# Performance work log

Hardware: AMD Instinct MI355X
Metric: run time of the kernel (lower is better)

Reference implementation:

```python
import jax, jax.numpy as jnp
import numpy as np

B, S, D, H = 2, 2048, 1024, 16
DK = D // H

def setup_inputs() -> dict:
    key = jax.random.key(0)
    ks = jax.random.split(key, 9)
    scale = 1.0 / np.sqrt(D)
    return {
        "x": jax.random.normal(ks[0], (B, S, D), dtype=jnp.float32),
        "Wq": jax.random.uniform(ks[1], (D, D), jnp.float32, -scale, scale),
        "bq": jax.random.uniform(ks[2], (D,), jnp.float32, -scale, scale),
        "Wk": jax.random.uniform(ks[3], (D, D), jnp.float32, -scale, scale),
        "bk": jax.random.uniform(ks[4], (D,), jnp.float32, -scale, scale),
        "Wv": jax.random.uniform(ks[5], (D, D), jnp.float32, -scale, scale),
        "bv": jax.random.uniform(ks[6], (D,), jnp.float32, -scale, scale),
        "Wo": jax.random.uniform(ks[7], (D, D), jnp.float32, -scale, scale),
        "bo": jax.random.uniform(ks[8], (D,), jnp.float32, -scale, scale),
    }

def reference(x, Wq, bq, Wk, bk, Wv, bv, Wo, bo):
    # QKV projections (torch Linear: x @ W.T + b)
    q = x @ Wq.T + bq
    k = x @ Wk.T + bk
    v = x @ Wv.T + bv
    # [B, H, S, DK]
    q = q.reshape(B, S, H, DK).transpose(0, 2, 1, 3)
    k = k.reshape(B, S, H, DK).transpose(0, 2, 1, 3)
    v = v.reshape(B, S, H, DK).transpose(0, 2, 1, 3)
    scores = jnp.einsum('bhqd,bhkd->bhqk', q, k) / jnp.sqrt(jnp.float32(DK))
    p = jax.nn.softmax(scores, axis=-1)  # dropout is identity in eval mode
    o = jnp.einsum('bhqk,bhkd->bhqd', p, v)
    o = o.transpose(0, 2, 1, 3).reshape(B, S, D)
    return o @ Wo.T + bo
```

## Files before the change

kernel.cpp:

```cpp
#include <hip/hip_runtime.h>
#include <hip/hip_bf16.h>


typedef __attribute__((ext_vector_type(8))) short short8;
typedef __attribute__((ext_vector_type(4))) short short4v;
typedef __attribute__((ext_vector_type(4))) float f32x4;
typedef __attribute__((ext_vector_type(8))) unsigned short u16x8;
typedef __attribute__((ext_vector_type(2))) unsigned int u32x2;

__device__ __forceinline__ unsigned short f2bf(float f) {
    unsigned int u = __builtin_bit_cast(unsigned int, f);
    u += 0x7FFFu + ((u >> 16) & 1u);
    return (unsigned short)(u >> 16);
}

__device__ __forceinline__ unsigned short bfc(float f) {
    return __builtin_bit_cast(unsigned short, __float2bfloat16(f));
}

__device__ __forceinline__ float exp2_fast(float x) {
    return __builtin_amdgcn_exp2f(x);
}

__device__ __forceinline__ void gload16(const void* gsrc, void* ldst) {
    __builtin_amdgcn_global_load_lds(
        (const __attribute__((address_space(1))) unsigned int*)gsrc,
        (__attribute__((address_space(3))) unsigned int*)ldst, 16, 0, 0);
}

__global__ void cast_all(const float* __restrict__ x,
                         const float* __restrict__ wq, const float* __restrict__ wk,
                         const float* __restrict__ wv, const float* __restrict__ wo,
                         unsigned short* __restrict__ xb,
                         unsigned short* __restrict__ wqb, unsigned short* __restrict__ wkb,
                         unsigned short* __restrict__ wvb, unsigned short* __restrict__ wob)
{
    const int z = blockIdx.y;
    const float* src; unsigned short* dst; int n4;
    if (z == 0)      { src = x;  dst = xb;  n4 = 4096 * 1024 / 4; }
    else if (z == 1) { src = wq; dst = wqb; n4 = 1024 * 1024 / 4; }
    else if (z == 2) { src = wk; dst = wkb; n4 = 1024 * 1024 / 4; }
    else if (z == 3) { src = wv; dst = wvb; n4 = 1024 * 1024 / 4; }
    else             { src = wo; dst = wob; n4 = 1024 * 1024 / 4; }
    int i = blockIdx.x * blockDim.x + threadIdx.x;
    if (i < n4) {
        float4 v = reinterpret_cast<const float4*>(src)[i];
        ushort4 o;
        o.x = f2bf(v.x); o.y = f2bf(v.y); o.z = f2bf(v.z); o.w = f2bf(v.w);
        reinterpret_cast<ushort4*>(dst)[i] = o;
    }
}

__global__ __launch_bounds__(256, 2)
void qkv_gemm(const unsigned short* __restrict__ A,
              const unsigned short* __restrict__ Wq_,
              const unsigned short* __restrict__ Wk_,
              const unsigned short* __restrict__ Wv_,
              const float* __restrict__ bq_,
              const float* __restrict__ bk_,
              const float* __restrict__ bv_,
              unsigned short* __restrict__ Qb,
              unsigned short* __restrict__ Kb,
              unsigned short* __restrict__ Vtb)
{
    const int K = 1024;
    __shared__ __align__(16) unsigned short As[128][64];
    __shared__ __align__(16) unsigned short Bs[128][64];

    const int z = blockIdx.z;
    const unsigned short* Bw = (z == 0) ? Wq_ : (z == 1) ? Wk_ : Wv_;
    const float* bias = (z == 0) ? bq_ : (z == 1) ? bk_ : bv_;
    unsigned short* dst = (z == 0) ? Qb : (z == 1) ? Kb : Vtb;
    const float alpha = (z == 0) ? 0.125f * 1.44269504088896340736f : 1.0f;

    const int tid  = threadIdx.x;
    const int lane = tid & 63;
    const int wave = tid >> 6;
    const int wm = (wave >> 1) * 64;
    const int wn = (wave & 1) * 64;
    const int rowBase = blockIdx.y * 128;
    const int colBase = blockIdx.x * 128;
    const int l15 = lane & 15;
    const int lg  = lane >> 4;

    const int srow   = lane >> 3;
    const int schunk = lane & 7;
    const int gchunk = schunk ^ srow;

    f32x4 acc[4][4] = {};

    for (int kt = 0; kt < K; kt += 64) {
        __syncthreads();
#pragma unroll
        for (int it = 0; it < 4; ++it) {
            int r = wave * 8 + it * 32 + srow;
            gload16(A  + (size_t)(rowBase + r) * K + kt + gchunk * 8, &As[wave * 8 + it * 32][0]);
            gload16(Bw + (size_t)(colBase + r) * K + kt + gchunk * 8, &Bs[wave * 8 + it * 32][0]);
        }
        __syncthreads();
#pragma unroll
        for (int kk = 0; kk < 2; ++kk) {
            short8 af[4], bf[4];
#pragma unroll
            for (int fm = 0; fm < 4; ++fm) {
                int r  = wm + fm * 16 + l15;
                int kb = (kk * 4 + lg) ^ (r & 7);
                af[fm] = *reinterpret_cast<const short8*>(&As[r][kb * 8]);
            }
#pragma unroll
            for (int fn = 0; fn < 4; ++fn) {
                int r  = wn + fn * 16 + l15;
                int kb = (kk * 4 + lg) ^ (r & 7);
                bf[fn] = *reinterpret_cast<const short8*>(&Bs[r][kb * 8]);
            }
#pragma unroll
            for (int fm = 0; fm < 4; ++fm)
#pragma unroll
                for (int fn = 0; fn < 4; ++fn)
                    acc[fm][fn] = __builtin_amdgcn_mfma_f32_16x16x32_bf16(
                        af[fm], bf[fn], acc[fm][fn], 0, 0, 0);
        }
    }

#pragma unroll
    for (int fm = 0; fm < 4; ++fm)
#pragma unroll
        for (int fn = 0; fn < 4; ++fn)
#pragma unroll
            for (int r = 0; r < 4; ++r) {
                int grow = rowBase + wm + fm * 16 + lg * 4 + r;
                int gcol = colBase + wn + fn * 16 + l15;
                float v = (acc[fm][fn][r] + bias[gcol]) * alpha;
                int b = grow >> 11, s = grow & 2047;
                int h = gcol >> 6,  dk = gcol & 63;
                if (z < 2)
                    dst[(((size_t)b * 16 + h) * 2048 + s) * 64 + dk] = f2bf(v);
                else
                    dst[(((size_t)b * 16 + h) * 64 + dk) * 2048 + s] = f2bf(v);
            }
}

__global__ __launch_bounds__(256, 2)
void gemm_out(const unsigned short* __restrict__ A,
              const unsigned short* __restrict__ Bw,
              const float* __restrict__ bias,
              float* __restrict__ Cout, int M, int N, int K)
{
    __shared__ __align__(16) unsigned short As[128][64];
    __shared__ __align__(16) unsigned short Bs[64][64];

    const int tid  = threadIdx.x;
    const int lane = tid & 63;
    const int wave = tid >> 6;
    const int wm = (wave >> 1) * 64;
    const int wn = (wave & 1) * 32;
    const int rowBase = blockIdx.y * 128;
    const int colBase = blockIdx.x * 64;
    const int l15 = lane & 15;
    const int lg  = lane >> 4;

    const int srow   = lane >> 3;
    const int schunk = lane & 7;
    const int gchunk = schunk ^ srow;

    f32x4 acc[4][2] = {};

    for (int kt = 0; kt < K; kt += 64) {
        __syncthreads();
#pragma unroll
        for (int it = 0; it < 4; ++it) {
            int r = wave * 8 + it * 32 + srow;
            gload16(A + (size_t)(rowBase + r) * K + kt + gchunk * 8, &As[wave * 8 + it * 32][0]);
        }
#pragma unroll
        for (int it = 0; it < 2; ++it) {
            int rb = wave * 16 + it * 8;
            int r  = rb + srow;
            gload16(Bw + (size_t)(colBase + r) * K + kt + gchunk * 8, &Bs[rb][0]);
        }
        __syncthreads();
#pragma unroll
        for (int kk = 0; kk < 2; ++kk) {
            short8 af[4], bf[2];
#pragma unroll
            for (int fm = 0; fm < 4; ++fm) {
                int r  = wm + fm * 16 + l15;
                int kb = (kk * 4 + lg) ^ (r & 7);
                af[fm] = *reinterpret_cast<const short8*>(&As[r][kb * 8]);
            }
#pragma unroll
            for (int fn = 0; fn < 2; ++fn) {
                int r  = wn + fn * 16 + l15;
                int kb = (kk * 4 + lg) ^ (r & 7);
                bf[fn] = *reinterpret_cast<const short8*>(&Bs[r][kb * 8]);
            }
#pragma unroll
            for (int fm = 0; fm < 4; ++fm)
#pragma unroll
                for (int fn = 0; fn < 2; ++fn)
                    acc[fm][fn] = __builtin_amdgcn_mfma_f32_16x16x32_bf16(
                        af[fm], bf[fn], acc[fm][fn], 0, 0, 0);
        }
    }

#pragma unroll
    for (int fm = 0; fm < 4; ++fm)
#pragma unroll
        for (int fn = 0; fn < 2; ++fn)
#pragma unroll
            for (int r = 0; r < 4; ++r) {
                int grow = rowBase + wm + fm * 16 + lg * 4 + r;
                int gcol = colBase + wn + fn * 16 + l15;
                Cout[(size_t)grow * N + gcol] = acc[fm][fn][r] + bias[gcol];
            }
}

__global__ __launch_bounds__(256, 2)
void attn_kernel(const unsigned short* __restrict__ Q,
                 const unsigned short* __restrict__ Kt,
                 const unsigned short* __restrict__ Vt,
                 unsigned short* __restrict__ O)
{
    __shared__ __align__(16) unsigned short Ks[2][128][64];
    __shared__ __align__(16) unsigned short Vs[2][64][128];
    __shared__ __align__(16) unsigned short Ps[4][32][64];

    const int lid = blockIdx.x + 16 * blockIdx.y;
    const int bh  = 4 * (lid & 7) + ((lid >> 3) & 3);
    const int qt  = lid >> 5;
    const int tid  = threadIdx.x;
    const int lane = tid & 63;
    const int w    = tid >> 6;
    const int l15 = lane & 15;
    const int lg  = lane >> 4;

    const unsigned short* Qbh = Q  + (size_t)bh * 2048 * 64;
    const unsigned short* Kbh = Kt + (size_t)bh * 2048 * 64;
    const unsigned short* Vbh = Vt + (size_t)bh * 64 * 2048;

    short8 qf[2][2];
#pragma unroll
    for (int fq = 0; fq < 2; ++fq)
#pragma unroll
        for (int kk = 0; kk < 2; ++kk) {
            int row = qt * 128 + w * 32 + fq * 16 + l15;
            qf[fq][kk] = *reinterpret_cast<const short8*>(
                Qbh + (size_t)row * 64 + kk * 32 + lg * 8);
        }

    short8 ones;
#pragma unroll
    for (int j = 0; j < 8; ++j) ones[j] = (short)0x3F80;

    f32x4 accO[2][4] = {};
    f32x4 accSum[2] = {};

    const int sr  = tid >> 3, skb = tid & 7;
    const int vr  = tid >> 4, vkb = tid & 15;

    unsigned short* PsW = &Ps[w][0][0];

    u16x8 kst[4], vst[4];
#pragma unroll
    for (int it = 0; it < 4; ++it)
        kst[it] = *reinterpret_cast<const u16x8*>(Kbh + (size_t)(sr + it * 32) * 64 + skb * 8);
#pragma unroll
    for (int it = 0; it < 4; ++it)
        vst[it] = *reinterpret_cast<const u16x8*>(Vbh + (size_t)(vr + it * 16) * 2048 + vkb * 8);

    int cur = 0;
    for (int t = 0; t < 16; ++t) {
#pragma unroll
        for (int it = 0; it < 4; ++it) {
            int r = sr + it * 32;
            *reinterpret_cast<u16x8*>(&Ks[cur][r][(skb ^ (r & 7)) * 8]) = kst[it];
        }
#pragma unroll
        for (int it = 0; it < 4; ++it) {
            int r = vr + it * 16;
            *reinterpret_cast<u16x8*>(&Vs[cur][r][(vkb ^ (r & 15)) * 8]) = vst[it];
        }
        __syncthreads();

        if (t < 15) {
#pragma unroll
            for (int it = 0; it < 4; ++it)
                kst[it] = *reinterpret_cast<const u16x8*>(
                    Kbh + (size_t)((t + 1) * 128 + sr + it * 32) * 64 + skb * 8);
#pragma unroll
            for (int it = 0; it < 4; ++it)
                vst[it] = *reinterpret_cast<const u16x8*>(
                    Vbh + (size_t)(vr + it * 16) * 2048 + (t + 1) * 128 + vkb * 8);
        }

        f32x4 accS[8][2] = {};
#pragma unroll
        for (int kk = 0; kk < 2; ++kk) {
            short8 kf[8];
#pragma unroll
            for (int fk = 0; fk < 8; ++fk) {
                int r  = fk * 16 + l15;
                int kb = (kk * 4 + lg) ^ (r & 7);
                kf[fk] = *reinterpret_cast<const short8*>(&Ks[cur][r][kb * 8]);
            }
#pragma unroll
            for (int fk = 0; fk < 8; ++fk)
#pragma unroll
                for (int fq = 0; fq < 2; ++fq)
                    accS[fk][fq] = __builtin_amdgcn_mfma_f32_16x16x32_bf16(
                        kf[fk], qf[fq][kk], accS[fk][fq], 0, 0, 0);
        }

#pragma unroll
        for (int hh = 0; hh < 2; ++hh) {
#pragma unroll
            for (int fq = 0; fq < 2; ++fq) {
                const int ql = fq * 16 + l15;
#pragma unroll
                for (int f2 = 0; f2 < 4; ++f2) {
                    int fk = hh * 4 + f2;
                    float p0 = exp2_fast(accS[fk][fq][0]);
                    float p1 = exp2_fast(accS[fk][fq][1]);
                    float p2 = exp2_fast(accS[fk][fq][2]);
                    float p3 = exp2_fast(accS[fk][fq][3]);
                    unsigned int lo = (unsigned int)bfc(p0) | ((unsigned int)bfc(p1) << 16);
                    unsigned int hi = (unsigned int)bfc(p2) | ((unsigned int)bfc(p3) << 16);
                    u32x2 tmp; tmp.x = lo; tmp.y = hi;
                    short4v pk = __builtin_bit_cast(short4v, tmp);
                    int c = (f2 * 2 + (lg >> 1)) ^ (ql & 7);
                    *reinterpret_cast<short4v*>(
                        reinterpret_cast<char*>(PsW) + ql * 128 + c * 16 + (lg & 1) * 8) = pk;
                }
            }
            asm volatile("" ::: "memory");

#pragma unroll
            for (int k2 = 0; k2 < 2; ++k2) {
                short8 pf[2], vf[4];
#pragma unroll
                for (int fq = 0; fq < 2; ++fq) {
                    int ql = fq * 16 + l15;
                    int c  = (k2 * 4 + lg) ^ (ql & 7);
                    pf[fq] = *reinterpret_cast<const short8*>(
                        reinterpret_cast<char*>(PsW) + ql * 128 + c * 16);
                }
#pragma unroll
                for (int fd = 0; fd < 4; ++fd) {
                    int row = fd * 16 + l15;
                    int kb  = ((hh * 2 + k2) * 4 + lg) ^ (row & 15);
                    vf[fd] = *reinterpret_cast<const short8*>(&Vs[cur][row][kb * 8]);
                }
#pragma unroll
                for (int fq = 0; fq < 2; ++fq) {
#pragma unroll
                    for (int fd = 0; fd < 4; ++fd)
                        accO[fq][fd] = __builtin_amdgcn_mfma_f32_16x16x32_bf16(
                            pf[fq], vf[fd], accO[fq][fd], 0, 0, 0);
                    accSum[fq] = __builtin_amdgcn_mfma_f32_16x16x32_bf16(
                        pf[fq], ones, accSum[fq], 0, 0, 0);
                }
            }
            asm volatile("" ::: "memory");
        }

        cur ^= 1;
    }

    const int b = bh >> 4, h = bh & 15;
#pragma unroll
    for (int fq = 0; fq < 2; ++fq)
#pragma unroll
        for (int r = 0; r < 4; ++r) {
            float linv = 1.0f / accSum[fq][r];
            int s = qt * 128 + w * 32 + fq * 16 + lg * 4 + r;
#pragma unroll
            for (int fd = 0; fd < 4; ++fd) {
                int dk = fd * 16 + l15;
                O[((size_t)b * 2048 + s) * 1024 + h * 64 + dk] = f2bf(accO[fq][fd][r] * linv);
            }
        }
}

extern "C" void kernel_launch(void* const* d_in, const int* in_sizes, int n_in,
                              void* d_out, int out_size, void* d_ws, size_t ws_size,
                              hipStream_t stream)
{
    const float* x  = (const float*)d_in[0];
    const float* Wq = (const float*)d_in[1];
    const float* bq = (const float*)d_in[2];
    const float* Wk = (const float*)d_in[3];
    const float* bk = (const float*)d_in[4];
    const float* Wv = (const float*)d_in[5];
    const float* bv = (const float*)d_in[6];
    const float* Wo = (const float*)d_in[7];
    const float* bo = (const float*)d_in[8];
    float* out = (float*)d_out;

    char* ws = (char*)d_ws;
    unsigned short* xb  = (unsigned short*)(ws);
    unsigned short* wqb = (unsigned short*)(ws + ((size_t)8  << 20));
    unsigned short* wkb = (unsigned short*)(ws + ((size_t)10 << 20));
    unsigned short* wvb = (unsigned short*)(ws + ((size_t)12 << 20));
    unsigned short* wob = (unsigned short*)(ws + ((size_t)14 << 20));
    unsigned short* Qb  = (unsigned short*)(ws + ((size_t)16 << 20));
    unsigned short* Kb  = (unsigned short*)(ws + ((size_t)24 << 20));
    unsigned short* Vtb = (unsigned short*)(ws + ((size_t)32 << 20));
    unsigned short* Ob  = (unsigned short*)(ws + ((size_t)40 << 20));

    cast_all<<<dim3(4096, 5), 256, 0, stream>>>(x, Wq, Wk, Wv, Wo,
                                                xb, wqb, wkb, wvb, wob);

    qkv_gemm<<<dim3(8, 32, 3), 256, 0, stream>>>(xb, wqb, wkb, wvb, bq, bk, bv,
                                                 Qb, Kb, Vtb);

    attn_kernel<<<dim3(16, 32), 256, 0, stream>>>(Qb, Kb, Vtb, Ob);

    gemm_out<<<dim3(16, 32), 256, 0, stream>>>(Ob, wob, bo, out, 4096, 1024, 1024);
}
```

Baseline: 113.4 us.

## Split attention KV range in two and merge partials in a reduce kernel

The attention grid gains a z-dimension of 2, so each block processes half of the key/value tiles. It writes unnormalized bf16 partial outputs and row sums to the workspace, and a new reduce kernel adds the two halves and normalizes before the output projection. This doubles the number of blocks to improve CU occupancy and parallelism. The K/V LDS staging drops from double-buffered to single-buffered with an extra barrier. The price is an additional kernel launch, extra global traffic for the partials, and bf16 rounding of unnormalized partials.

```diff
diff --git a/kernel.cpp b/kernel.cpp
--- a/kernel.cpp
+++ b/kernel.cpp
@@ -12,6 +12,11 @@
     unsigned int u = __builtin_bit_cast(unsigned int, f);
     u += 0x7FFFu + ((u >> 16) & 1u);
     return (unsigned short)(u >> 16);
+}
+
+__device__ __forceinline__ float bf2f(unsigned short u) {
+    unsigned int v = (unsigned int)u << 16;
+    return __builtin_bit_cast(float, v);
 }
 
 __device__ __forceinline__ unsigned short bfc(float f) {
@@ -219,15 +224,18 @@
 void attn_kernel(const unsigned short* __restrict__ Q,
                  const unsigned short* __restrict__ Kt,
                  const unsigned short* __restrict__ Vt,
-                 unsigned short* __restrict__ O)
-{
-    __shared__ __align__(16) unsigned short Ks[2][128][64];
-    __shared__ __align__(16) unsigned short Vs[2][64][128];
+                 unsigned short* __restrict__ Op0,
+                 unsigned short* __restrict__ Op1,
+                 float* __restrict__ Lp)
+{
+    __shared__ __align__(16) unsigned short Ks[128][64];
+    __shared__ __align__(16) unsigned short Vs[64][128];
     __shared__ __align__(16) unsigned short Ps[4][32][64];
 
     const int lid = blockIdx.x + 16 * blockIdx.y;
     const int bh  = 4 * (lid & 7) + ((lid >> 3) & 3);
     const int qt  = lid >> 5;
+    const int kvh = blockIdx.z;
     const int tid  = threadIdx.x;
     const int lane = tid & 63;
     const int w    = tid >> 6;
@@ -237,6 +245,7 @@
     const unsigned short* Qbh = Q  + (size_t)bh * 2048 * 64;
     const unsigned short* Kbh = Kt + (size_t)bh * 2048 * 64;
     const unsigned short* Vbh = Vt + (size_t)bh * 64 * 2048;
+    unsigned short* Op = kvh ? Op1 : Op0;
 
     short8 qf[2][2];
 #pragma unroll
@@ -259,30 +268,34 @@
     const int vr  = tid >> 4, vkb = tid & 15;
 
     unsigned short* PsW = &Ps[w][0][0];
+    const int tbase = kvh * 8;
 
     u16x8 kst[4], vst[4];
 #pragma unroll
     for (int it = 0; it < 4; ++it)
-        kst[it] = *reinterpret_cast<const u16x8*>(Kbh + (size_t)(sr + it * 32) * 64 + skb * 8);
+        kst[it] = *reinterpret_cast<const u16x8*>(
+            Kbh + (size_t)(tbase * 128 + sr + it * 32) * 64 + skb * 8);
 #pragma unroll
     for (int it = 0; it < 4; ++it)
-        vst[it] = *reinterpret_cast<const u16x8*>(Vbh + (size_t)(vr + it * 16) * 2048 + vkb * 8);
-
-    int cur = 0;
-    for (int t = 0; t < 16; ++t) {
+        vst[it] = *reinterpret_cast<const u16x8*>(
+            Vbh + (size_t)(vr + it * 16) * 2048 + tbase * 128 + vkb * 8);
+
+    for (int tt = 0; tt < 8; ++tt) {
+        const int t = tbase + tt;
+        __syncthreads();
 #pragma unroll
         for (int it = 0; it < 4; ++it) {
             int r = sr + it * 32;
-            *reinterpret_cast<u16x8*>(&Ks[cur][r][(skb ^ (r & 7)) * 8]) = kst[it];
+            *reinterpret_cast<u16x8*>(&Ks[r][(skb ^ (r & 7)) * 8]) = kst[it];
         }
 #pragma unroll
         for (int it = 0; it < 4; ++it) {
             int r = vr + it * 16;
-            *reinterpret_cast<u16x8*>(&Vs[cur][r][(vkb ^ (r & 15)) * 8]) = vst[it];
-        }
-        __syncthreads();
-
-        if (t < 15) {
+            *reinterpret_cast<u16x8*>(&Vs[r][(vkb ^ (r & 15)) * 8]) = vst[it];
+        }
+        __syncthreads();
+
+        if (tt < 7) {
 #pragma unroll
             for (int it = 0; it < 4; ++it)
                 kst[it] = *reinterpret_cast<const u16x8*>(
@@ -301,7 +314,7 @@
             for (int fk = 0; fk < 8; ++fk) {
                 int r  = fk * 16 + l15;
                 int kb = (kk * 4 + lg) ^ (r & 7);
-                kf[fk] = *reinterpret_cast<const short8*>(&Ks[cur][r][kb * 8]);
+                kf[fk] = *reinterpret_cast<const short8*>(&Ks[r][kb * 8]);
             }
 #pragma unroll
             for (int fk = 0; fk < 8; ++fk)
@@ -348,7 +361,7 @@
                 for (int fd = 0; fd < 4; ++fd) {
                     int row = fd * 16 + l15;
                     int kb  = ((hh * 2 + k2) * 4 + lg) ^ (row & 15);
-                    vf[fd] = *reinterpret_cast<const short8*>(&Vs[cur][row][kb * 8]);
+                    vf[fd] = *reinterpret_cast<const short8*>(&Vs[row][kb * 8]);
                 }
 #pragma unroll
                 for (int fq = 0; fq < 2; ++fq) {
@@ -362,23 +375,46 @@
             }
             asm volatile("" ::: "memory");
         }
-
-        cur ^= 1;
     }
 
-    const int b = bh >> 4, h = bh & 15;
 #pragma unroll
     for (int fq = 0; fq < 2; ++fq)
 #pragma unroll
         for (int r = 0; r < 4; ++r) {
-            float linv = 1.0f / accSum[fq][r];
             int s = qt * 128 + w * 32 + fq * 16 + lg * 4 + r;
+            if (l15 == 0)
+                Lp[(size_t)kvh * 65536 + bh * 2048 + s] = accSum[fq][r];
 #pragma unroll
             for (int fd = 0; fd < 4; ++fd) {
                 int dk = fd * 16 + l15;
-                O[((size_t)b * 2048 + s) * 1024 + h * 64 + dk] = f2bf(accO[fq][fd][r] * linv);
-            }
-        }
+                Op[((size_t)(bh * 2048 + s)) * 64 + dk] = f2bf(accO[fq][fd][r]);
+            }
+        }
+}
+
+__global__ void reduce_kernel(const unsigned short* __restrict__ Op0,
+                              const unsigned short* __restrict__ Op1,
+                              const float* __restrict__ Lp,
+                              unsigned short* __restrict__ Ob)
+{
+    int gid = blockIdx.x * 256 + threadIdx.x;
+    size_t o = (size_t)gid * 8;
+    int row = (int)(o >> 10);
+    int col = (int)(o & 1023);
+    int h = col >> 6, dk0 = col & 63;
+    int b = row >> 11, s = row & 2047;
+    int bh = b * 16 + h;
+    size_t pidx = ((size_t)(bh * 2048 + s)) * 64 + dk0;
+
+    u16x8 a = *reinterpret_cast<const u16x8*>(Op0 + pidx);
+    u16x8 c = *reinterpret_cast<const u16x8*>(Op1 + pidx);
+    float l = Lp[bh * 2048 + s] + Lp[65536 + bh * 2048 + s];
+    float inv = 1.0f / l;
+    u16x8 out;
+#pragma unroll
+    for (int j = 0; j < 8; ++j)
+        out[j] = f2bf((bf2f(a[j]) + bf2f(c[j])) * inv);
+    *reinterpret_cast<u16x8*>(Ob + o) = out;
 }
 
 extern "C" void kernel_launch(void* const* d_in, const int* in_sizes, int n_in,
@@ -405,7 +441,10 @@
     unsigned short* Qb  = (unsigned short*)(ws + ((size_t)16 << 20));
     unsigned short* Kb  = (unsigned short*)(ws + ((size_t)24 << 20));
     unsigned short* Vtb = (unsigned short*)(ws + ((size_t)32 << 20));
-    unsigned short* Ob  = (unsigned short*)(ws + ((size_t)40 << 20));
+    unsigned short* Op1 = (unsigned short*)(ws + ((size_t)40 << 20));
+    unsigned short* Op0 = (unsigned short*)(ws);
+    float*          Lp  = (float*)(ws + ((size_t)8 << 20));
+    unsigned short* Obf = (unsigned short*)(ws + ((size_t)16 << 20));
 
     cast_all<<<dim3(4096, 5), 256, 0, stream>>>(x, Wq, Wk, Wv, Wo,
                                                 xb, wqb, wkb, wvb, wob);
@@ -413,7 +452,9 @@
     qkv_gemm<<<dim3(8, 32, 3), 256, 0, stream>>>(xb, wqb, wkb, wvb, bq, bk, bv,
                                                  Qb, Kb, Vtb);
 
-    attn_kernel<<<dim3(16, 32), 256, 0, stream>>>(Qb, Kb, Vtb, Ob);
-
-    gemm_out<<<dim3(16, 32), 256, 0, stream>>>(Ob, wob, bo, out, 4096, 1024, 1024);
-}
+    attn_kernel<<<dim3(16, 32, 2), 256, 0, stream>>>(Qb, Kb, Vtb, Op0, Op1, Lp);
+
+    reduce_kernel<<<2048, 256, 0, stream>>>(Op0, Op1, Lp, Obf);
+
+    gemm_out<<<dim3(16, 32), 256, 0, stream>>>(Obf, wob, bo, out, 4096, 1024, 1024);
+}
```

Result: slower. 119.9 us (+5.7%).
